# Optimization experiments

Hardware: AMD Instinct MI355X
Metric: run time of the kernel (lower is better)

Reference implementation:

```python
import jax, jax.numpy as jnp
import numpy as np

# ---- static dims ----
B, L, V = 8, 512, 100000
E, NERD, COREFD = 100, 20, 20          # word / ner / coref embedding dims
H, DIS, REL, HT = 128, 20, 97, 512     # hidden, dis embed, relations, n_pairs
W, N, R, C = 512, 32, 8, 256           # DNC word len, cells, read heads, ctrl hidden
IN_SIZE = E + NERD + COREFD            # 140 == H + 12 (required by final_layer)
DNC_OUT = H + 12                        # 140
CTRL_IN = IN_SIZE + R * W               # 4236
MASK_MIN, EPS, CLIP = 0.1, 1e-6, 20.0
# interface vector layout: read keys, read strengths, write key, write strength,
# erase, write vec, free gates, alloc gate, write gate, read modes,
# write mask, read masks, fwd sharpness, bwd sharpness
XI_SIZES = [R*W, R, W, 1, W, W, R, 1, 1, 3*R, W, R*W, R, R]
XI = sum(XI_SIZES)


def setup_inputs():
    key = jax.random.key(0)
    ks = iter(jax.random.split(key, 40))
    def nrm(shape, s=0.02):
        return (jax.random.normal(next(ks), shape) * s).astype(jnp.float32)
    def ri(shape, hi):
        return jax.random.randint(next(ks), shape, 0, hi)
    return dict(
        context_idxs=ri((B, L), V),
        pos=ri((B, L), L),
        context_ner=ri((B, L), 7),
        context_char_idxs=ri((B, L, 16), 262),
        context_lens=jnp.full((B,), L, dtype=jnp.int32),
        h_mapping=jax.random.uniform(next(ks), (B, HT, L), jnp.float32) / L,
        t_mapping=jax.random.uniform(next(ks), (B, HT, L), jnp.float32) / L,
        relation_mask=jnp.ones((B, HT), jnp.float32),
        dis_h_2_t=ri((B, HT), 20),
        dis_t_2_h=ri((B, HT), 20),
        word_emb=nrm((V, E), 0.1),
        entity_emb=nrm((L, COREFD), 0.1),
        ner_emb=nrm((7, NERD), 0.1),
        dis_emb=nrm((20, DIS), 0.1),
        Wih0=nrm((CTRL_IN, 4*C)), Whh0=nrm((C, 4*C)), b0=jnp.zeros((4*C,), jnp.float32),
        Wih1=nrm((C, 4*C)), Whh1=nrm((C, 4*C)), b1=jnp.zeros((4*C,), jnp.float32),
        Wih2=nrm((C, 4*C)), Whh2=nrm((C, 4*C)), b2=jnp.zeros((4*C,), jnp.float32),
        W_xi=nrm((C, XI)), b_xi=jnp.zeros((XI,), jnp.float32),
        W_out=nrm((C + R*W, DNC_OUT)), b_out=jnp.zeros((DNC_OUT,), jnp.float32),
        W_final=nrm((DNC_OUT, 2*H)), b_final=jnp.zeros((2*H,), jnp.float32),
        W_re=nrm((2*H, H)), b_re=jnp.zeros((H,), jnp.float32),
        W_bili=nrm((REL, H+DIS, H+DIS)), b_bili=jnp.zeros((REL,), jnp.float32),
    )


def _lstm(x, h, c, Wih, Whh, b):
    z = x @ Wih + h @ Whh + b
    i, f, g, o = jnp.split(z, 4, axis=-1)
    c = jax.nn.sigmoid(f) * c + jax.nn.sigmoid(i) * jnp.tanh(g)
    h = jax.nn.sigmoid(o) * jnp.tanh(c)
    return h, c


def _content(M, key_, beta, mask):
    # M [B,N,W]; key_, mask [B,h,W]; beta [B,h] -> weights [B,h,N]
    k = key_ * mask
    Mm = M[:, None] * mask[:, :, None]                 # [B,h,N,W]
    dot = jnp.einsum('bhw,bhnw->bhn', k, Mm)
    kn = jnp.linalg.norm(k, axis=-1)[..., None]
    Mn = jnp.linalg.norm(Mm, axis=-1)
    cos = dot / (kn * Mn + EPS)
    return jax.nn.softmax(beta[..., None] * cos, axis=-1)


def _sharpen(w, s):
    w = (w + EPS) ** s[..., None]
    return w / w.sum(-1, keepdims=True)


def _dnc(x, params):
    (Wih0, Whh0, b0, Wih1, Whh1, b1, Wih2, Whh2, b2, W_xi, b_xi, W_out, b_out) = params
    Bs = x.shape[0]
    eye = jnp.eye(N, dtype=x.dtype)
    splits = np.cumsum(XI_SIZES)[:-1]

    def step(carry, x_t):
        (h0, c0, h1, c1, h2, c2, M, u, wr, ww, p, Lnk, reads) = carry
        ci = jnp.concatenate([x_t, reads.reshape(Bs, R*W)], -1)
        h0, c0 = _lstm(ci, h0, c0, Wih0, Whh0, b0)
        h1, c1 = _lstm(h0, h1, c1, Wih1, Whh1, b1)
        h2, c2 = _lstm(h1, h2, c2, Wih2, Whh2, b2)
        h = jnp.clip(h2, -CLIP, CLIP)
        xi = h @ W_xi + b_xi
        (rk, rb, wk, wb, er, wv, fg, ga, gw, rm,
         wmask, rmask, sf, sb) = jnp.split(xi, splits, axis=-1)
        rk = rk.reshape(Bs, R, W)
        rb = 1 + jax.nn.softplus(rb)                    # [B,R]
        wk = wk.reshape(Bs, 1, W)
        wb = 1 + jax.nn.softplus(wb)                    # [B,1]
        er = jax.nn.sigmoid(er)                         # [B,W]
        fg = jax.nn.sigmoid(fg)                         # [B,R]
        ga = jax.nn.sigmoid(ga)
        gw = jax.nn.sigmoid(gw)
        pi = jax.nn.softmax(rm.reshape(Bs, R, 3), -1)
        wmask = MASK_MIN + (1 - MASK_MIN) * jax.nn.sigmoid(wmask)
        rmask = MASK_MIN + (1 - MASK_MIN) * jax.nn.sigmoid(rmask).reshape(Bs, R, W)
        sf = 1 + jax.nn.softplus(sf)
        sb = 1 + jax.nn.softplus(sb)

        # retention / usage
        psi = jnp.prod(1 - fg[:, :, None] * wr, axis=1)  # [B,N]
        u = (u + ww - u * ww) * psi
        # allocation weighting via sorted free list
        order = jnp.argsort(u, axis=-1)
        us = jnp.take_along_axis(u, order, -1)
        cp = jnp.cumprod(jnp.concatenate([jnp.ones((Bs, 1), u.dtype), us[:, :-1]], -1), -1)
        a_s = (1 - us) * cp
        a = jnp.zeros_like(u).at[jnp.arange(Bs)[:, None], order].set(a_s)
        # write addressing (masked content + allocation)
        cw = _content(M, wk, wb, wmask[:, None, :])[:, 0]
        ww = gw * (ga * a + (1 - ga) * cw)
        # de-allocate content of freed cells, then write
        M = M * psi[:, :, None]
        M = M * (1 - ww[:, :, None] * er[:, None, :]) + ww[:, :, None] * wv[:, None, :]
        # temporal link matrix (uses previous precedence p)
        Lnk = (1 - ww[:, :, None] - ww[:, None, :]) * Lnk + ww[:, :, None] * p[:, None, :]
        Lnk = Lnk * (1 - eye)
        p = (1 - ww.sum(-1, keepdims=True)) * p + ww
        # read addressing with link sharpness control
        fw = _sharpen(jnp.einsum('bij,brj->bri', Lnk, wr), sf)
        bw = _sharpen(jnp.einsum('bji,brj->bri', Lnk, wr), sb)
        cr = _content(M, rk, rb, rmask)
        wr = pi[..., 0:1] * bw + pi[..., 1:2] * cr + pi[..., 2:3] * fw
        reads = jnp.einsum('brn,bnw->brw', wr, M)
        y = jnp.concatenate([h, reads.reshape(Bs, R*W)], -1) @ W_out + b_out
        return (h0, c0, h1, c1, h2, c2, M, u, wr, ww, p, Lnk, reads), y

    z = jnp.zeros
    carry0 = (z((Bs, C)), z((Bs, C)), z((Bs, C)), z((Bs, C)), z((Bs, C)), z((Bs, C)),
              z((Bs, N, W)), z((Bs, N)), z((Bs, R, N)), z((Bs, N)), z((Bs, N)),
              z((Bs, N, N)), z((Bs, R, W)))
    _, ys = jax.lax.scan(step, carry0, x.transpose(1, 0, 2))
    return ys.transpose(1, 0, 2)  # [B,L,DNC_OUT]


def reference(context_idxs, pos, context_ner, context_char_idxs, context_lens,
              h_mapping, t_mapping, relation_mask, dis_h_2_t, dis_t_2_h,
              word_emb, entity_emb, ner_emb, dis_emb,
              Wih0, Whh0, b0, Wih1, Whh1, b1, Wih2, Whh2, b2,
              W_xi, b_xi, W_out, b_out, W_final, b_final, W_re, b_re,
              W_bili, b_bili):
    sent = jnp.concatenate([word_emb[context_idxs], entity_emb[pos],
                            ner_emb[context_ner]], -1)      # [B,L,140]
    dnc_params = (Wih0, Whh0, b0, Wih1, Whh1, b1, Wih2, Whh2, b2,
                  W_xi, b_xi, W_out, b_out)
    out = _dnc(sent, dnc_params)                             # [B,L,140]
    out = out @ W_final + b_final                            # LockedDropout: identity (eval)
    ctx = jax.nn.relu(out @ W_re + b_re)                     # [B,L,H]
    s0 = jnp.einsum('bpl,blh->bph', h_mapping, ctx)
    t0 = jnp.einsum('bpl,blh->bph', t_mapping, ctx)
    s_rep = jnp.concatenate([s0, dis_emb[dis_h_2_t]], -1)    # [B,P,148]
    t_rep = jnp.concatenate([t0, dis_emb[dis_t_2_h]], -1)
    return jnp.einsum('bpi,kij,bpj->bpk', s_rep, W_bili, t_rep) + b_bili
```

## Files before the change

kernel.cpp:

```cpp
#include <hip/hip_runtime.h>
#include <math.h>

#define B8      8
#define LSEQ    512
#define NWG     256
#define TPB     512
#define RELK    97
#define BI      148
#define FSTR    16

#define oWA     0
#define oW1     18432
#define oW2     20480
#define oWX     22528
#define oWY     34816
#define oST     37196
#define LDSF    40948
#define LDSB    (LDSF*4)

__device__ __forceinline__ float sigf(float x){
  return (x >= 0.f) ? 1.f/(1.f + expf(-x)) : expf(x)/(1.f + expf(x));
}
__device__ __forceinline__ float spf(float x){
  return (x > 0.f) ? x + log1pf(expf(-x)) : log1pf(expf(x));
}
__device__ __forceinline__ float agld(const float* p){
  return __hip_atomic_load(p, __ATOMIC_RELAXED, __HIP_MEMORY_SCOPE_AGENT);
}
__device__ __forceinline__ void agst(float* p, float v){
  __hip_atomic_store(p, v, __ATOMIC_RELAXED, __HIP_MEMORY_SCOPE_AGENT);
}

__global__ __launch_bounds__(256)
void k_sent(const int* __restrict__ cidx, const int* __restrict__ pos,
            const int* __restrict__ ner, const float* __restrict__ wemb,
            const float* __restrict__ eemb, const float* __restrict__ nemb,
            float* __restrict__ sent)
{
  int flat = blockIdx.x*256 + threadIdx.x;
  if (flat >= B8*LSEQ*140) return;
  int d = flat % 140; int bl = flat / 140;
  float v;
  if (d < 100)      v = wemb[(size_t)cidx[bl]*100 + d];
  else if (d < 120) v = eemb[(size_t)pos[bl]*20 + (d-100)];
  else              v = nemb[(size_t)ner[bl]*20 + (d-120)];
  sent[flat] = v;
}

__global__ __launch_bounds__(256)
void k_tr(const float* __restrict__ A, const float* __restrict__ Bsrc,
          int N, int K1a, int K1b, int K2, long long total, float* __restrict__ T)
{
  long long i = (long long)blockIdx.x*256 + threadIdx.x;
  if (i >= total) return;
  int k = (int)(i % K2);
  long long c = i / K2;
  float v = 0.f;
  if (k < K1a)            v = A[(size_t)k*N + c];
  else if (k < K1a+K1b)   v = Bsrc[(size_t)(k-K1a)*N + c];
  T[i] = v;
}

__device__ __forceinline__ void gbar(int* flags, int* genrep, int seq){
  __syncthreads();
  const int tid = threadIdx.x;
  const int bid = blockIdx.x;
  if (tid == 0){
    asm volatile("s_waitcnt vmcnt(0)" ::: "memory");
    __hip_atomic_store(&flags[bid*FSTR], seq, __ATOMIC_RELAXED, __HIP_MEMORY_SCOPE_AGENT);
  }
  if (bid == 0){
    if (tid < NWG){
      while (__hip_atomic_load(&flags[tid*FSTR], __ATOMIC_RELAXED, __HIP_MEMORY_SCOPE_AGENT) < seq)
        __builtin_amdgcn_s_sleep(1);
    }
    __syncthreads();
    if (tid < NWG)
      __hip_atomic_store(&genrep[tid*FSTR], seq, __ATOMIC_RELAXED, __HIP_MEMORY_SCOPE_AGENT);
  } else if (tid == 0){
    while (__hip_atomic_load(&genrep[bid*FSTR], __ATOMIC_RELAXED, __HIP_MEMORY_SCOPE_AGENT) < seq)
      __builtin_amdgcn_s_sleep(1);
  }
  __syncthreads();
}

__device__ void mem_phase(float* lds, const float* __restrict__ xi,
                          float* __restrict__ M, float* u_g, float* ww_g,
                          float* p_g, float* wr_g, float* L_g, float* rout)
{
  const int tid = threadIdx.x;
  float* mL  = lds;
  float* mwr = lds+1024;
  float* mwrn= lds+1280;
  float* mcr = lds+1536;
  float* mfw = lds+1792;
  float* mbw = lds+2048;
  float* PSI = lds+2304;
  float* UU  = lds+2336;
  float* US  = lds+2368;
  float* AA  = lds+2400;
  float* CW  = lds+2432;
  float* WWN = lds+2464;
  float* WWO = lds+2496;
  float* PP  = lds+2528;
  int*   mord= (int*)(lds+2560);
  float* mh  = lds+2592;
  float* mpi = lds+2624;
  float* msc = lds+2648;
  float* q1  = lds+2688;
  float* q2  = lds+3200;

  if (tid < 8){
    mh[tid]    = 1.f + spf(agld(&xi[4096+tid]));
    mh[8+tid]  = 1.f + spf(agld(&xi[10283+tid]));
    mh[16+tid] = 1.f + spf(agld(&xi[10291+tid]));
    mh[24+tid] = sigf(agld(&xi[5641+tid]));
    float e0=agld(&xi[5651+3*tid]), e1=agld(&xi[5652+3*tid]), e2=agld(&xi[5653+3*tid]);
    float mx=fmaxf(e0,fmaxf(e1,e2));
    float x0=expf(e0-mx), x1=expf(e1-mx), x2=expf(e2-mx);
    float inv=1.f/(x0+x1+x2);
    mpi[tid*3]=x0*inv; mpi[tid*3+1]=x1*inv; mpi[tid*3+2]=x2*inv;
  }
  if (tid==0){ msc[0]=1.f+spf(agld(&xi[4616])); msc[1]=sigf(agld(&xi[5649])); msc[2]=sigf(agld(&xi[5650])); }
  if (tid<32){ UU[tid]=u_g[tid]; WWO[tid]=ww_g[tid]; PP[tid]=p_g[tid]; }
  if (tid<256) mwr[tid]=wr_g[tid];
  mL[tid]=L_g[tid]; mL[tid+512]=L_g[tid+512];
  { float wm = 0.1f+0.9f*sigf(agld(&xi[5675+tid])); q1[tid]=agld(&xi[4104+tid])*wm; q2[tid]=wm; }
  __syncthreads();

  if (tid<32){
    float psi=1.f;
    #pragma unroll
    for (int r=0;r<8;r++) psi *= (1.f - mh[24+r]*mwr[r*32+tid]);
    PSI[tid]=psi;
    float uo=UU[tid], wo=WWO[tid];
    UU[tid]=(uo+wo-uo*wo)*psi;
  }
  __syncthreads();
  if (tid<32){
    float un=UU[tid]; int rank=0;
    for (int m=0;m<32;m++){ float um=UU[m]; rank += (um<un)||(um==un && m<tid); }
    mord[rank]=tid;
  }
  __syncthreads();
  if (tid<32) US[tid]=UU[mord[tid]];
  __syncthreads();
  if (tid==0){ float cp=1.f; for (int j=0;j<32;j++){ AA[mord[j]]=(1.f-US[j])*cp; cp*=US[j]; } }
  __syncthreads();

  { float q=q1[tid]*q1[tid];
    for (int o=32;o;o>>=1) q += __shfl_down(q,o,64);
    if ((tid&63)==0) msc[8+(tid>>6)]=q; }
  __syncthreads();
  if (tid==0){ float q=0.f; for (int i=0;i<8;i++) q+=msc[8+i]; msc[3]=sqrtf(q); }
  __syncthreads();
  { int n=tid>>4, wsub=tid&15;
    float d=0.f,q=0.f;
    for (int i=0;i<32;i++){ int w=wsub+16*i; float m=M[(size_t)n*512+w]; float t2=m*q2[w]; d+=q1[w]*t2; q+=t2*t2; }
    for (int o=8;o;o>>=1){ d+=__shfl_down(d,o,16); q+=__shfl_down(q,o,16); }
    if (wsub==0){ float cs=d/(msc[3]*sqrtf(q)+1e-6f); CW[n]=msc[0]*cs; } }
  __syncthreads();
  if (tid==0){ float mx=-1e30f; for(int n=0;n<32;n++) mx=fmaxf(mx,CW[n]); msc[4]=mx; }
  __syncthreads();
  if (tid<32) CW[tid]=expf(CW[tid]-msc[4]);
  __syncthreads();
  if (tid==0){ float sm=0.f; for(int n=0;n<32;n++) sm+=CW[n]; msc[5]=1.f/sm; }
  __syncthreads();
  if (tid<32) CW[tid]*=msc[5];
  __syncthreads();
  if (tid<32) WWN[tid]=msc[2]*(msc[1]*AA[tid]+(1.f-msc[1])*CW[tid]);
  __syncthreads();
  { float er=sigf(agld(&xi[4617+tid])); float wv=agld(&xi[5129+tid]);
    for (int n=0;n<32;n++){ size_t idx=(size_t)n*512+tid; float m=M[idx];
      M[idx]=m*PSI[n]*(1.f-WWN[n]*er)+WWN[n]*wv; } }
  __syncthreads();
  for (int ii=0;ii<2;ii++){ int f=tid+512*ii; int i=f>>5, j=f&31;
    float nl=(1.f-WWN[i]-WWN[j])*mL[f]+WWN[i]*PP[j];
    mL[f]=(i==j)?0.f:nl; }
  __syncthreads();
  if (tid==0){ float sw=0.f; for(int n=0;n<32;n++) sw+=WWN[n]; msc[6]=sw; }
  __syncthreads();
  if (tid<32) PP[tid]=(1.f-msc[6])*PP[tid]+WWN[tid];
  __syncthreads();
  { int r=(tid>>5)&7, i=tid&31; bool isB=(tid>=256);
    float accv=0.f;
    if (!isB){ for (int j=0;j<32;j++) accv += mL[i*32+j]*mwr[r*32+j]; }
    else     { for (int j=0;j<32;j++) accv += mL[j*32+i]*mwr[r*32+j]; }
    float sp = isB? mh[16+r] : mh[8+r];
    float e = expf(sp*logf(accv+1e-6f));
    if (!isB) mfw[r*32+i]=e; else mbw[r*32+i]=e; }
  __syncthreads();
  if (tid<16){ int r=tid&7; float sm=0.f;
    if (tid<8){ for(int n=0;n<32;n++) sm+=mfw[r*32+n]; msc[16+r]=1.f/sm; }
    else      { for(int n=0;n<32;n++) sm+=mbw[r*32+n]; msc[24+r]=1.f/sm; } }
  __syncthreads();
  { int r=(tid>>5)&7, i=tid&31; bool isB=(tid>=256);
    if (!isB) mfw[r*32+i]*=msc[16+r]; else mbw[r*32+i]*=msc[24+r]; }
  __syncthreads();
  for (int r=0;r<8;r++){
    { float rm=0.1f+0.9f*sigf(agld(&xi[6187+r*512+tid]));
      q1[tid]=agld(&xi[r*512+tid])*rm; q2[tid]=rm; }
    __syncthreads();
    { float q=q1[tid]*q1[tid];
      for (int o=32;o;o>>=1) q+=__shfl_down(q,o,64);
      if ((tid&63)==0) msc[8+(tid>>6)]=q; }
    __syncthreads();
    if (tid==0){ float qq=0.f; for(int i=0;i<8;i++) qq+=msc[8+i]; msc[32]=sqrtf(qq); }
    __syncthreads();
    { int n=tid>>4, wsub=tid&15;
      float d=0.f,q=0.f;
      for (int i=0;i<32;i++){ int w=wsub+16*i; float m=M[(size_t)n*512+w]; float t2=m*q2[w]; d+=q1[w]*t2; q+=t2*t2; }
      for (int o=8;o;o>>=1){ d+=__shfl_down(d,o,16); q+=__shfl_down(q,o,16); }
      if (wsub==0){ float cs=d/(msc[32]*sqrtf(q)+1e-6f); mcr[r*32+n]=mh[r]*cs; } }
    __syncthreads();
  }
  if (tid<8){ int r=tid; float mx=-1e30f;
    for (int n=0;n<32;n++) mx=fmaxf(mx,mcr[r*32+n]);
    float sm=0.f;
    for (int n=0;n<32;n++){ float e=expf(mcr[r*32+n]-mx); mcr[r*32+n]=e; sm+=e; }
    float inv=1.f/sm;
    for (int n=0;n<32;n++) mcr[r*32+n]*=inv; }
  __syncthreads();
  if (tid<256){ int r=tid>>5, n=tid&31;
    float v=mpi[r*3]*mbw[r*32+n]+mpi[r*3+1]*mcr[r*32+n]+mpi[r*3+2]*mfw[r*32+n];
    mwrn[tid]=v; wr_g[tid]=v; }
  __syncthreads();
  { int r=tid>>6, wsub=tid&63;
    for (int i2=0;i2<8;i2++){ int w=wsub+64*i2;
      float accv=0.f;
      for (int n=0;n<32;n++) accv+=mwrn[r*32+n]*M[(size_t)n*512+w];
      agst(&rout[r*512+w], accv); } }
  if (tid<32){ u_g[tid]=UU[tid]; ww_g[tid]=WWN[tid]; p_g[tid]=PP[tid]; }
  L_g[tid]=mL[tid]; L_g[tid+512]=mL[tid+512];
}

__global__ __launch_bounds__(TPB, 1)
void dnc_persist(
  const float* __restrict__ sent,
  const float* __restrict__ Wih0, const float* __restrict__ Whh0, const float* __restrict__ b0,
  const float* __restrict__ Wih1, const float* __restrict__ Whh1, const float* __restrict__ b1,
  const float* __restrict__ Wih2, const float* __restrict__ Whh2, const float* __restrict__ b2,
  const float* __restrict__ WXIT, const float* __restrict__ bxi,
  const float* __restrict__ Wout, const float* __restrict__ bout,
  float* __restrict__ yh,
  float* __restrict__ reads,
  float* __restrict__ h0, float* __restrict__ h1,
  float* __restrict__ h2u, float* __restrict__ h2c,
  float* __restrict__ c0p, float* __restrict__ c1p, float* __restrict__ c2p,
  float* __restrict__ zp0, float* __restrict__ zp1, float* __restrict__ zp2,
  float* __restrict__ yp, float* __restrict__ xig,
  float* __restrict__ Mb, float* __restrict__ ug, float* __restrict__ wwg,
  float* __restrict__ pg, float* __restrict__ wrg, float* __restrict__ Lg,
  int* flags, int* genrep)
{
  extern __shared__ float lds[];
  const int wg  = blockIdx.x;
  const int tid = threadIdx.x;
  const int cg  = wg >> 4, kg  = wg & 15;
  const int cgB = wg >> 3, kgB = wg & 7;
  const int ycg = wg >> 6, ykg = wg & 63;
  const int xc  = tid >> 6, xk = tid & 63;
  float* stg = lds + oST;
  int seq = 0;

  for (int f=tid; f<18432; f+=TPB){
    int kk=f>>6, cc=f&63;
    int gk=kg*288+kk, gc=cg*64+cc;
    float v=0.f;
    if (gk<4236) v=Wih0[(size_t)gk*1024+gc];
    else if (gk<4492) v=Whh0[(size_t)(gk-4236)*1024+gc];
    lds[oWA+f]=v;
  }
  for (int f=tid; f<2048; f+=TPB){
    int kk=f>>5, cc=f&31;
    int gk=kgB*64+kk, gc=cgB*32+cc;
    lds[oW1+f] = (gk<256)? Wih1[(size_t)gk*1024+gc] : Whh1[(size_t)(gk-256)*1024+gc];
  }
  for (int f=tid; f<2048; f+=TPB){
    int kk=f>>5, cc=f&31;
    int gk=kgB*64+kk, gc=cgB*32+cc;
    lds[oW2+f] = (gk<256)? Wih2[(size_t)gk*1024+gc] : Whh2[(size_t)(gk-256)*1024+gc];
  }
  for (int f=tid; f<12288; f+=TPB){
    int cl=f>>8, k=f&255; int col=wg*48+cl;
    lds[oWX+f] = (col<10299)? WXIT[(size_t)col*256+k] : 0.f;
  }
  for (int f=tid; f<2380; f+=TPB){
    int kk=f/35, cc=f%35;
    int gk=ykg*68+kk, gc=ycg*35+cc;
    lds[oWY+f] = Wout[(size_t)gk*140+gc];
  }
  __syncthreads();

  #pragma unroll 1
  for (int t=0; t<LSEQ; t++){
    {
      float* sAct = stg;
      float* sActY= stg+2304;
      for (int f=tid; f<2304; f+=TPB){
        int s=f/288, kk=f%288; int g=kg*288+kk;
        float v;
        if (g<140)       v = sent[((size_t)s*512+t)*140+g];
        else if (g<4236) v = agld(&reads[s*4096+g-140]);
        else if (g<4492) v = agld(&h0[s*256+(g-4236)]);
        else             v = 0.f;
        sAct[f]=v;
      }
      if (t>0) for (int f=tid; f<544; f+=TPB){
        int s=f/68, kk=f%68; int gy=ykg*68+kk;
        sActY[f] = (gy<256)? agld(&h2c[s*256+gy]) : agld(&reads[s*4096+gy-256]);
      }
      __syncthreads();
      { int cc=tid&63, s=tid>>6;
        const float* wAl = lds+oWA;
        const float* ac  = sAct + s*288;
        float acc=0.f;
        #pragma unroll 8
        for (int kk=0; kk<288; kk++) acc += wAl[kk*64+cc]*ac[kk];
        agst(&zp0[(size_t)(kg*8+s)*1024 + cg*64+cc], acc); }
      if (t>0 && tid<280){ int s=tid/35, cc=tid%35;
        const float* wYl = lds+oWY;
        const float* ac  = sActY + s*68;
        float acc=0.f;
        #pragma unroll 4
        for (int kk=0; kk<68; kk++) acc += wYl[kk*35+cc]*ac[kk];
        agst(&yp[(size_t)(ykg*8+s)*144 + ycg*35+cc], acc); }
    }
    gbar(flags,genrep,++seq);

    if (wg < 64){
      int s = wg>>3, part = wg&7;
      float* sP = stg;
      { int j32=tid&31, q=(tid>>5)&3, kp=tid>>7;
        int col = q*256 + part*32 + j32;
        float v=0.f;
        for (int k2=kp*4; k2<kp*4+4; k2++) v += agld(&zp0[(size_t)(k2*8+s)*1024+col]);
        sP[kp*128 + q*32 + j32] = v; }
      __syncthreads();
      if (tid<32){
        int j = part*32 + tid;
        float zq[4];
        #pragma unroll
        for (int q=0;q<4;q++){ float v=0.f;
          for (int k2=0;k2<4;k2++) v += sP[k2*128+q*32+tid];
          zq[q]=v + b0[q*256+j]; }
        float cold=c0p[s*256+j];
        float cn=sigf(zq[1])*cold + sigf(zq[0])*tanhf(zq[2]);
        float h=sigf(zq[3])*tanhf(cn);
        c0p[s*256+j]=cn;
        agst(&h0[s*256+j], h);
      }
    }
    gbar(flags,genrep,++seq);

    {
      float* sAct = stg;
      for (int f=tid; f<512; f+=TPB){ int s=f>>6, kk=f&63; int g=kgB*64+kk;
        sAct[f] = (g<256)? agld(&h0[s*256+g]) : agld(&h1[s*256+g-256]); }
      __syncthreads();
      if (tid<256){ int cc=tid&31, s=tid>>5;
        const float* w1l = lds+oW1;
        const float* ac  = sAct + s*64;
        float acc=0.f;
        #pragma unroll 8
        for (int kk=0; kk<64; kk++) acc += w1l[kk*32+cc]*ac[kk];
        agst(&zp1[(size_t)(kgB*8+s)*1024 + cgB*32+cc], acc); }
    }
    gbar(flags,genrep,++seq);

    if (wg < 64){
      int s = wg>>3, part = wg&7;
      float* sP = stg;
      if (tid<256){ int j32=tid&31, q=(tid>>5)&3, kp=tid>>7;
        int col = q*256 + part*32 + j32;
        float v=0.f;
        for (int k2=kp*4; k2<kp*4+4; k2++) v += agld(&zp1[(size_t)(k2*8+s)*1024+col]);
        sP[kp*128 + q*32 + j32] = v; }
      __syncthreads();
      if (tid<32){
        int j = part*32 + tid;
        float zq[4];
        #pragma unroll
        for (int q=0;q<4;q++) zq[q]=sP[q*32+tid]+sP[128+q*32+tid]+b1[q*256+j];
        float cold=c1p[s*256+j];
        float cn=sigf(zq[1])*cold + sigf(zq[0])*tanhf(zq[2]);
        float h=sigf(zq[3])*tanhf(cn);
        c1p[s*256+j]=cn;
        agst(&h1[s*256+j], h);
      }
    }
    gbar(flags,genrep,++seq);

    {
      float* sAct = stg;
      for (int f=tid; f<512; f+=TPB){ int s=f>>6, kk=f&63; int g=kgB*64+kk;
        sAct[f] = (g<256)? agld(&h1[s*256+g]) : agld(&h2u[s*256+g-256]); }
      __syncthreads();
      if (tid<256){ int cc=tid&31, s=tid>>5;
        const float* w2l = lds+oW2;
        const float* ac  = sAct + s*64;
        float acc=0.f;
        #pragma unroll 8
        for (int kk=0; kk<64; kk++) acc += w2l[kk*32+cc]*ac[kk];
        agst(&zp2[(size_t)(kgB*8+s)*1024 + cgB*32+cc], acc); }
    }
    gbar(flags,genrep,++seq);

    if (wg < 64){
      int s = wg>>3, part = wg&7;
      float* sP = stg;
      if (tid<256){ int j32=tid&31, q=(tid>>5)&3, kp=tid>>7;
        int col = q*256 + part*32 + j32;
        float v=0.f;
        for (int k2=kp*4; k2<kp*4+4; k2++) v += agld(&zp2[(size_t)(k2*8+s)*1024+col]);
        sP[kp*128 + q*32 + j32] = v; }
      __syncthreads();
      if (tid<32){
        int j = part*32 + tid;
        float zq[4];
        #pragma unroll
        for (int q=0;q<4;q++) zq[q]=sP[q*32+tid]+sP[128+q*32+tid]+b2[q*256+j];
        float cold=c2p[s*256+j];
        float cn=sigf(zq[1])*cold + sigf(zq[0])*tanhf(zq[2]);
        float h2=sigf(zq[3])*tanhf(cn);
        float hc=fminf(fmaxf(h2,-20.f),20.f);
        c2p[s*256+j]=cn;
        agst(&h2u[s*256+j], h2);
        agst(&h2c[s*256+j], hc);
      }
    }
    gbar(flags,genrep,++seq);

    {
      float* sA2 = stg;
      for (int f=tid; f<2048; f+=TPB){ int s=f>>8, j=f&255;
        sA2[s*260+j] = agld(&h2c[s*256+j]); }
      __syncthreads();
      float accx[6][8];
      #pragma unroll
      for (int cc=0;cc<6;cc++)
        #pragma unroll
        for (int s=0;s<8;s++) accx[cc][s]=0.f;
      #pragma unroll
      for (int s=0;s<8;s++){
        float4 a = *reinterpret_cast<const float4*>(&sA2[s*260 + (xk<<2)]);
        #pragma unroll
        for (int cc=0;cc<6;cc++){
          float4 wv = *reinterpret_cast<const float4*>(&lds[oWX + (xc*6+cc)*256 + (xk<<2)]);
          accx[cc][s] += a.x*wv.x + a.y*wv.y + a.z*wv.z + a.w*wv.w;
        }
      }
      #pragma unroll
      for (int o=32;o;o>>=1)
        #pragma unroll
        for (int cc=0;cc<6;cc++)
          #pragma unroll
          for (int s=0;s<8;s++) accx[cc][s]+=__shfl_down(accx[cc][s],o,64);
      if ((tid&63)==0){
        #pragma unroll
        for (int cc=0;cc<6;cc++){
          int col = wg*48 + xc*6 + cc;
          if (col < 10299){
            #pragma unroll
            for (int s=0;s<8;s++) agst(&xig[(size_t)s*10299+col], accx[cc][s]+bxi[col]);
          }
        }
      }
    }
    gbar(flags,genrep,++seq);

    if (wg < 8){
      mem_phase(stg, xig + (size_t)wg*10299, Mb + (size_t)wg*16384,
                ug+wg*32, wwg+wg*32, pg+wg*32, wrg+wg*256, Lg+wg*1024,
                reads + wg*4096);
    } else if (wg < 148 && t > 0){
      int ty = t-1, j = wg-8;
      int s = tid>>6, kg2 = tid&63;
      float v = agld(&yp[(size_t)(kg2*8+s)*144 + j]);
      #pragma unroll
      for (int o=32;o;o>>=1) v += __shfl_down(v,o,64);
      if (kg2==0) yh[((size_t)s*512+ty)*140+j] = v + bout[j];
    }
    gbar(flags,genrep,++seq);
  }

  {
    float* sActY = stg;
    for (int f=tid; f<544; f+=TPB){
      int s=f/68, kk=f%68; int gy=ykg*68+kk;
      sActY[f] = (gy<256)? agld(&h2c[s*256+gy]) : agld(&reads[s*4096+gy-256]);
    }
    __syncthreads();
    if (tid<280){ int s=tid/35, cc=tid%35;
      const float* wYl = lds+oWY;
      const float* ac  = sActY + s*68;
      float acc=0.f;
      for (int kk=0; kk<68; kk++) acc += wYl[kk*35+cc]*ac[kk];
      agst(&yp[(size_t)(ykg*8+s)*144 + ycg*35+cc], acc); }
  }
  gbar(flags,genrep,++seq);
  if (wg>=8 && wg<148){
    int j = wg-8;
    int s = tid>>6, kg2 = tid&63;
    float v = agld(&yp[(size_t)(kg2*8+s)*144 + j]);
    #pragma unroll
    for (int o=32;o;o>>=1) v += __shfl_down(v,o,64);
    if (kg2==0) yh[((size_t)s*512+511)*140+j] = v + bout[j];
  }
}

__global__ __launch_bounds__(256)
void gemm16(int M, int N, int K,
            const float* __restrict__ A, long long sAb, int lda,
            const float* __restrict__ Bm, long long sBb, int ldb,
            float* __restrict__ C, long long sCb, int ldc,
            const float* __restrict__ bias, int relu)
{
  __shared__ float sAh[16*512];
  const int tid = threadIdx.x;
  const float* Ab = A + (size_t)blockIdx.y*sAb;
  const float* Bb = Bm + (size_t)blockIdx.y*sBb;
  float* Cb = C + (size_t)blockIdx.y*sCb;
  const int m0 = blockIdx.x*16;
  const int tot = 16*K;
  for (int f = tid; f < tot; f += 256) sAh[f] = Ab[(size_t)m0*lda + f];
  __syncthreads();
  int c = (tid & 63)*4; int rg = tid >> 6;
  if (c >= N) return;
  float acc[4][4] = {};
  for (int k=0;k<K;k++){
    float4 bv = *reinterpret_cast<const float4*>(Bb + (size_t)k*ldb + c);
    #pragma unroll
    for (int rr=0;rr<4;rr++){
      float a = sAh[(rg*4+rr)*K + k];
      acc[rr][0] += a*bv.x; acc[rr][1] += a*bv.y; acc[rr][2] += a*bv.z; acc[rr][3] += a*bv.w;
    }
  }
  for (int rr=0;rr<4;rr++){
    int m = m0 + rg*4 + rr;
    #pragma unroll
    for (int e=0;e<4;e++){
      float v = acc[rr][e] + (bias ? bias[c+e] : 0.f);
      if (relu) v = fmaxf(v, 0.f);
      Cb[(size_t)m*ldc + c + e] = v;
    }
  }
}

__global__ __launch_bounds__(256)
void bilin(const float* __restrict__ s0, const float* __restrict__ t0,
           const float* __restrict__ dis_emb, const int* __restrict__ dht,
           const int* __restrict__ dth, const float* __restrict__ Wb,
           const float* __restrict__ bb, float* __restrict__ out)
{
  __shared__ float sS[BI][33];
  __shared__ float sT[32][152];
  const int tid = threadIdx.x;
  const int bp0 = blockIdx.x*32;
  for (int f = tid; f < 32*BI; f += 256){
    int pp = f / BI, i = f % BI;
    int bp = bp0 + pp;
    float sv, tv;
    if (i < 128){ sv = s0[(size_t)bp*128 + i]; tv = t0[(size_t)bp*128 + i]; }
    else {
      sv = dis_emb[(size_t)dht[bp]*20 + (i-128)];
      tv = dis_emb[(size_t)dth[bp]*20 + (i-128)];
    }
    sS[i][pp] = sv; sT[pp][i] = tv;
  }
  __syncthreads();
  const int ppg = tid >> 5, jb = tid & 31;
  const int pp0 = ppg*4;
  const int k0 = blockIdx.y*49, kend = min(k0+49, RELK);
  for (int k = k0; k < kend; k++){
    const float* Wk = Wb + (size_t)k*BI*BI;
    float acc[4][5];
    #pragma unroll
    for (int a=0;a<4;a++) for (int b=0;b<5;b++) acc[a][b]=0.f;
    for (int i=0;i<BI;i++){
      float sv0 = sS[i][pp0], sv1 = sS[i][pp0+1], sv2 = sS[i][pp0+2], sv3 = sS[i][pp0+3];
      const float* wrow = Wk + i*BI;
      #pragma unroll
      for (int jj=0;jj<5;jj++){
        int j = jb + 32*jj;
        if (j < BI){
          float w = wrow[j];
          acc[0][jj] += sv0*w; acc[1][jj] += sv1*w; acc[2][jj] += sv2*w; acc[3][jj] += sv3*w;
        }
      }
    }
    float dot[4] = {0.f,0.f,0.f,0.f};
    #pragma unroll
    for (int jj=0;jj<5;jj++){
      int j = jb + 32*jj;
      if (j < BI){
        #pragma unroll
        for (int p4=0;p4<4;p4++) dot[p4] += acc[p4][jj]*sT[pp0+p4][j];
      }
    }
    #pragma unroll
    for (int p4=0;p4<4;p4++)
      for (int o=16;o;o>>=1) dot[p4] += __shfl_down(dot[p4], o, 32);
    if (jb == 0){
      #pragma unroll
      for (int p4=0;p4<4;p4++)
        out[(size_t)(bp0+pp0+p4)*RELK + k] = dot[p4] + bb[k];
    }
  }
}

extern "C" void kernel_launch(void* const* d_in, const int* in_sizes, int n_in,
                              void* d_out, int out_size, void* d_ws, size_t ws_size,
                              hipStream_t stream)
{
  (void)in_sizes; (void)n_in; (void)out_size; (void)ws_size;
  const int*   ctx_idx = (const int*)  d_in[0];
  const int*   pos     = (const int*)  d_in[1];
  const int*   nerI    = (const int*)  d_in[2];
  const float* h_map   = (const float*)d_in[5];
  const float* t_map   = (const float*)d_in[6];
  const int*   dht     = (const int*)  d_in[8];
  const int*   dth     = (const int*)  d_in[9];
  const float* wemb    = (const float*)d_in[10];
  const float* eemb    = (const float*)d_in[11];
  const float* nemb    = (const float*)d_in[12];
  const float* demb    = (const float*)d_in[13];
  const float* Wih0    = (const float*)d_in[14];
  const float* Whh0    = (const float*)d_in[15];
  const float* b0      = (const float*)d_in[16];
  const float* Wih1    = (const float*)d_in[17];
  const float* Whh1    = (const float*)d_in[18];
  const float* b1      = (const float*)d_in[19];
  const float* Wih2    = (const float*)d_in[20];
  const float* Whh2    = (const float*)d_in[21];
  const float* b2      = (const float*)d_in[22];
  const float* Wxi     = (const float*)d_in[23];
  const float* bxi     = (const float*)d_in[24];
  const float* Wout    = (const float*)d_in[25];
  const float* bout    = (const float*)d_in[26];
  const float* Wfin    = (const float*)d_in[27];
  const float* bfin    = (const float*)d_in[28];
  const float* Wre     = (const float*)d_in[29];
  const float* bre     = (const float*)d_in[30];
  const float* Wbili   = (const float*)d_in[31];
  const float* bbili   = (const float*)d_in[32];

  float* ws    = (float*)d_ws;
  float* sent  = ws;
  float* yh    = sent + 573440;
  float* o256  = yh + 573440;
  float* s0b   = o256 + 1048576;
  float* t0b   = s0b + 524288;
  float* SB    = t0b + 524288;
  float* reads = SB + 0;
  float* h0    = SB + 32768;
  float* h1    = SB + 34816;
  float* h2u   = SB + 36864;
  float* h2c   = SB + 38912;
  float* c0p   = SB + 40960;
  float* c1p   = SB + 43008;
  float* c2p   = SB + 45056;
  float* zp0   = SB + 47104;
  float* zp1   = SB + 178176;
  float* zp2   = SB + 243712;
  float* yp    = SB + 309248;
  float* xig   = SB + 382976;
  float* Mb    = SB + 465368;
  float* ug    = SB + 596440;
  float* wwg   = SB + 596696;
  float* pg    = SB + 596952;
  float* wrg   = SB + 597208;
  float* Lg    = SB + 599256;
  float* barf  = SB + 607448;
  float* SEnd  = SB + 615640;
  float* WXIT  = SEnd;
  float* ctxb  = yh;
  int* flags  = (int*)barf;
  int* genrep = flags + 256*FSTR;

  hipMemsetAsync(SB, 0, (size_t)615640*sizeof(float), stream);

  hipLaunchKernelGGL(k_tr, dim3(10299), dim3(256), 0, stream,
                     Wxi, Wxi, 10299, 256, 0, 256, (long long)2636544, WXIT);
  hipLaunchKernelGGL(k_sent, dim3((573440+255)/256), dim3(256), 0, stream,
                     ctx_idx, pos, nerI, wemb, eemb, nemb, sent);

  hipFuncSetAttribute(reinterpret_cast<const void*>(dnc_persist),
                      hipFuncAttributeMaxDynamicSharedMemorySize, LDSB);

  hipLaunchKernelGGL(dnc_persist, dim3(NWG), dim3(TPB), LDSB, stream,
                     sent, Wih0, Whh0, b0, Wih1, Whh1, b1, Wih2, Whh2, b2,
                     WXIT, bxi, Wout, bout, yh, reads,
                     h0, h1, h2u, h2c, c0p, c1p, c2p,
                     zp0, zp1, zp2, yp, xig,
                     Mb, ug, wwg, pg, wrg, Lg, flags, genrep);

  hipLaunchKernelGGL(gemm16, dim3(256,1), dim3(256), 0, stream,
                     4096, 256, 140, yh, (long long)0, 140, Wfin, (long long)0, 256,
                     o256, (long long)0, 256, bfin, 0);
  hipLaunchKernelGGL(gemm16, dim3(256,1), dim3(256), 0, stream,
                     4096, 128, 256, o256, (long long)0, 256, Wre, (long long)0, 128,
                     ctxb, (long long)0, 128, bre, 1);
  hipLaunchKernelGGL(gemm16, dim3(32,8), dim3(256), 0, stream,
                     512, 128, 512, h_map, (long long)(512*512), 512,
                     ctxb, (long long)(512*128), 128,
                     s0b, (long long)(512*128), 128, (const float*)nullptr, 0);
  hipLaunchKernelGGL(gemm16, dim3(32,8), dim3(256), 0, stream,
                     512, 128, 512, t_map, (long long)(512*512), 512,
                     ctxb, (long long)(512*128), 128,
                     t0b, (long long)(512*128), 128, (const float*)nullptr, 0);
  hipLaunchKernelGGL(bilin, dim3(128,2), dim3(256), 0, stream,
                     s0b, t0b, demb, dht, dth, Wbili, bbili, (float*)d_out);
}
```

Measured before the change: 90.09 ms.

## Fuse LSTM layer 1/2 matvec with gate update per workgroup, cutting grid barriers

Each workgroup now owns one hidden unit across all four gates. It keeps the layer-1 and layer-2 weight columns in registers and computes the full dot product with wave shuffle reductions. This removes the partial-sum buffers zp1/zp2 and two grid-wide barriers per timestep. Layer-0 gate reduction also moves to shuffles across all 256 workgroups. h1/h2u are double-buffered to avoid read/write races, and the barrier spin sleep is lengthened. The cost is 64 extra VGPRs per thread for the weights and a larger sleep granularity, which may add barrier wake-up latency.

```diff
diff --git a/kernel.cpp b/kernel.cpp
--- a/kernel.cpp
+++ b/kernel.cpp
@@ -10,12 +10,10 @@
 #define FSTR    16
 
 #define oWA     0
-#define oW1     18432
-#define oW2     20480
-#define oWX     22528
-#define oWY     34816
-#define oST     37196
-#define LDSF    40948
+#define oWX     18432
+#define oWY     30720
+#define oST     33100
+#define LDSF    36852
 #define LDSB    (LDSF*4)
 
 __device__ __forceinline__ float sigf(float x){
@@ -72,14 +70,14 @@
   if (bid == 0){
     if (tid < NWG){
       while (__hip_atomic_load(&flags[tid*FSTR], __ATOMIC_RELAXED, __HIP_MEMORY_SCOPE_AGENT) < seq)
-        __builtin_amdgcn_s_sleep(1);
+        __builtin_amdgcn_s_sleep(8);
     }
     __syncthreads();
     if (tid < NWG)
       __hip_atomic_store(&genrep[tid*FSTR], seq, __ATOMIC_RELAXED, __HIP_MEMORY_SCOPE_AGENT);
   } else if (tid == 0){
     while (__hip_atomic_load(&genrep[bid*FSTR], __ATOMIC_RELAXED, __HIP_MEMORY_SCOPE_AGENT) < seq)
-      __builtin_amdgcn_s_sleep(1);
+      __builtin_amdgcn_s_sleep(8);
   }
   __syncthreads();
 }
@@ -247,7 +245,7 @@
   float* __restrict__ h0, float* __restrict__ h1,
   float* __restrict__ h2u, float* __restrict__ h2c,
   float* __restrict__ c0p, float* __restrict__ c1p, float* __restrict__ c2p,
-  float* __restrict__ zp0, float* __restrict__ zp1, float* __restrict__ zp2,
+  float* __restrict__ zp0,
   float* __restrict__ yp, float* __restrict__ xig,
   float* __restrict__ Mb, float* __restrict__ ug, float* __restrict__ wwg,
   float* __restrict__ pg, float* __restrict__ wrg, float* __restrict__ Lg,
@@ -257,9 +255,9 @@
   const int wg  = blockIdx.x;
   const int tid = threadIdx.x;
   const int cg  = wg >> 4, kg  = wg & 15;
-  const int cgB = wg >> 3, kgB = wg & 7;
   const int ycg = wg >> 6, ykg = wg & 63;
   const int xc  = tid >> 6, xk = tid & 63;
+  const int lane = tid & 63, sw = tid >> 6;
   float* stg = lds + oST;
   int seq = 0;
 
@@ -271,16 +269,6 @@
     else if (gk<4492) v=Whh0[(size_t)(gk-4236)*1024+gc];
     lds[oWA+f]=v;
   }
-  for (int f=tid; f<2048; f+=TPB){
-    int kk=f>>5, cc=f&31;
-    int gk=kgB*64+kk, gc=cgB*32+cc;
-    lds[oW1+f] = (gk<256)? Wih1[(size_t)gk*1024+gc] : Whh1[(size_t)(gk-256)*1024+gc];
-  }
-  for (int f=tid; f<2048; f+=TPB){
-    int kk=f>>5, cc=f&31;
-    int gk=kgB*64+kk, gc=cgB*32+cc;
-    lds[oW2+f] = (gk<256)? Wih2[(size_t)gk*1024+gc] : Whh2[(size_t)(gk-256)*1024+gc];
-  }
   for (int f=tid; f<12288; f+=TPB){
     int cl=f>>8, k=f&255; int col=wg*48+cl;
     lds[oWX+f] = (col<10299)? WXIT[(size_t)col*256+k] : 0.f;
@@ -290,10 +278,28 @@
     int gk=ykg*68+kk, gc=ycg*35+cc;
     lds[oWY+f] = Wout[(size_t)gk*140+gc];
   }
+  float w1r[32], w2r[32];
+  #pragma unroll
+  for (int g=0; g<4; g++)
+    #pragma unroll
+    for (int i=0; i<8; i++){
+      int kk = lane + 64*i;
+      w1r[g*8+i] = (kk<256)? Wih1[(size_t)kk*1024 + g*256+wg]
+                           : Whh1[(size_t)(kk-256)*1024 + g*256+wg];
+      w2r[g*8+i] = (kk<256)? Wih2[(size_t)kk*1024 + g*256+wg]
+                           : Whh2[(size_t)(kk-256)*1024 + g*256+wg];
+    }
+  float bb0[4], bb1[4], bb2[4];
+  #pragma unroll
+  for (int g=0; g<4; g++){
+    bb0[g]=b0[g*256+wg]; bb1[g]=b1[g*256+wg]; bb2[g]=b2[g*256+wg];
+  }
   __syncthreads();
 
   #pragma unroll 1
   for (int t=0; t<LSEQ; t++){
+    const int hb = t&1, hw = hb^1;
+
     {
       float* sAct = stg;
       float* sActY= stg+2304;
@@ -328,105 +334,79 @@
     }
     gbar(flags,genrep,++seq);
 
-    if (wg < 64){
-      int s = wg>>3, part = wg&7;
-      float* sP = stg;
-      { int j32=tid&31, q=(tid>>5)&3, kp=tid>>7;
-        int col = q*256 + part*32 + j32;
-        float v=0.f;
-        for (int k2=kp*4; k2<kp*4+4; k2++) v += agld(&zp0[(size_t)(k2*8+s)*1024+col]);
-        sP[kp*128 + q*32 + j32] = v; }
-      __syncthreads();
-      if (tid<32){
-        int j = part*32 + tid;
-        float zq[4];
-        #pragma unroll
-        for (int q=0;q<4;q++){ float v=0.f;
-          for (int k2=0;k2<4;k2++) v += sP[k2*128+q*32+tid];
-          zq[q]=v + b0[q*256+j]; }
-        float cold=c0p[s*256+j];
-        float cn=sigf(zq[1])*cold + sigf(zq[0])*tanhf(zq[2]);
-        float h=sigf(zq[3])*tanhf(cn);
-        c0p[s*256+j]=cn;
-        agst(&h0[s*256+j], h);
+    {
+      int g = lane>>4, p = lane&15;
+      float val = agld(&zp0[(size_t)(p*8+sw)*1024 + g*256 + wg]);
+      #pragma unroll
+      for (int o=8;o;o>>=1) val += __shfl_down(val,o,16);
+      float zi=__shfl(val, 0,64), zf=__shfl(val,16,64);
+      float zg=__shfl(val,32,64), zo=__shfl(val,48,64);
+      if (lane==0){
+        zi+=bb0[0]; zf+=bb0[1]; zg+=bb0[2]; zo+=bb0[3];
+        float cold=c0p[sw*256+wg];
+        float cn=sigf(zf)*cold + sigf(zi)*tanhf(zg);
+        float h=sigf(zo)*tanhf(cn);
+        c0p[sw*256+wg]=cn;
+        agst(&h0[sw*256+wg], h);
       }
     }
     gbar(flags,genrep,++seq);
 
     {
-      float* sAct = stg;
-      for (int f=tid; f<512; f+=TPB){ int s=f>>6, kk=f&63; int g=kgB*64+kk;
-        sAct[f] = (g<256)? agld(&h0[s*256+g]) : agld(&h1[s*256+g-256]); }
-      __syncthreads();
-      if (tid<256){ int cc=tid&31, s=tid>>5;
-        const float* w1l = lds+oW1;
-        const float* ac  = sAct + s*64;
-        float acc=0.f;
-        #pragma unroll 8
-        for (int kk=0; kk<64; kk++) acc += w1l[kk*32+cc]*ac[kk];
-        agst(&zp1[(size_t)(kgB*8+s)*1024 + cgB*32+cc], acc); }
+      const float* h1r = h1 + (size_t)hb*2048;
+      float a[8];
+      #pragma unroll
+      for (int i=0;i<8;i++){
+        int k = lane + 64*i;
+        a[i] = (i<4)? agld(&h0[sw*256+k]) : agld(&h1r[sw*256+k-256]);
+      }
+      float acc[4]={0.f,0.f,0.f,0.f};
+      #pragma unroll
+      for (int i=0;i<8;i++)
+        #pragma unroll
+        for (int g=0;g<4;g++) acc[g] += a[i]*w1r[g*8+i];
+      #pragma unroll
+      for (int o=32;o;o>>=1)
+        #pragma unroll
+        for (int g=0;g<4;g++) acc[g]+=__shfl_down(acc[g],o,64);
+      if (lane==0){
+        float zi=acc[0]+bb1[0], zf=acc[1]+bb1[1], zg=acc[2]+bb1[2], zo=acc[3]+bb1[3];
+        float cold=c1p[sw*256+wg];
+        float cn=sigf(zf)*cold + sigf(zi)*tanhf(zg);
+        float h=sigf(zo)*tanhf(cn);
+        c1p[sw*256+wg]=cn;
+        agst(&h1[(size_t)hw*2048 + sw*256+wg], h);
+      }
     }
     gbar(flags,genrep,++seq);
 
-    if (wg < 64){
-      int s = wg>>3, part = wg&7;
-      float* sP = stg;
-      if (tid<256){ int j32=tid&31, q=(tid>>5)&3, kp=tid>>7;
-        int col = q*256 + part*32 + j32;
-        float v=0.f;
-        for (int k2=kp*4; k2<kp*4+4; k2++) v += agld(&zp1[(size_t)(k2*8+s)*1024+col]);
-        sP[kp*128 + q*32 + j32] = v; }
-      __syncthreads();
-      if (tid<32){
-        int j = part*32 + tid;
-        float zq[4];
-        #pragma unroll
-        for (int q=0;q<4;q++) zq[q]=sP[q*32+tid]+sP[128+q*32+tid]+b1[q*256+j];
-        float cold=c1p[s*256+j];
-        float cn=sigf(zq[1])*cold + sigf(zq[0])*tanhf(zq[2]);
-        float h=sigf(zq[3])*tanhf(cn);
-        c1p[s*256+j]=cn;
-        agst(&h1[s*256+j], h);
-      }
-    }
-    gbar(flags,genrep,++seq);
-
     {
-      float* sAct = stg;
-      for (int f=tid; f<512; f+=TPB){ int s=f>>6, kk=f&63; int g=kgB*64+kk;
-        sAct[f] = (g<256)? agld(&h1[s*256+g]) : agld(&h2u[s*256+g-256]); }
-      __syncthreads();
-      if (tid<256){ int cc=tid&31, s=tid>>5;
-        const float* w2l = lds+oW2;
-        const float* ac  = sAct + s*64;
-        float acc=0.f;
-        #pragma unroll 8
-        for (int kk=0; kk<64; kk++) acc += w2l[kk*32+cc]*ac[kk];
-        agst(&zp2[(size_t)(kgB*8+s)*1024 + cgB*32+cc], acc); }
-    }
-    gbar(flags,genrep,++seq);
-
-    if (wg < 64){
-      int s = wg>>3, part = wg&7;
-      float* sP = stg;
-      if (tid<256){ int j32=tid&31, q=(tid>>5)&3, kp=tid>>7;
-        int col = q*256 + part*32 + j32;
-        float v=0.f;
-        for (int k2=kp*4; k2<kp*4+4; k2++) v += agld(&zp2[(size_t)(k2*8+s)*1024+col]);
-        sP[kp*128 + q*32 + j32] = v; }
-      __syncthreads();
-      if (tid<32){
-        int j = part*32 + tid;
-        float zq[4];
-        #pragma unroll
-        for (int q=0;q<4;q++) zq[q]=sP[q*32+tid]+sP[128+q*32+tid]+b2[q*256+j];
-        float cold=c2p[s*256+j];
-        float cn=sigf(zq[1])*cold + sigf(zq[0])*tanhf(zq[2]);
-        float h2=sigf(zq[3])*tanhf(cn);
+      const float* h1c = h1 + (size_t)hw*2048;
+      const float* h2r = h2u + (size_t)hb*2048;
+      float a[8];
+      #pragma unroll
+      for (int i=0;i<8;i++){
+        int k = lane + 64*i;
+        a[i] = (i<4)? agld(&h1c[sw*256+k]) : agld(&h2r[sw*256+k-256]);
+      }
+      float acc[4]={0.f,0.f,0.f,0.f};
+      #pragma unroll
+      for (int i=0;i<8;i++)
+        #pragma unroll
+        for (int g=0;g<4;g++) acc[g] += a[i]*w2r[g*8+i];
+      #pragma unroll
+      for (int o=32;o;o>>=1)
+        #pragma unroll
+        for (int g=0;g<4;g++) acc[g]+=__shfl_down(acc[g],o,64);
+      if (lane==0){
+        float zi=acc[0]+bb2[0], zf=acc[1]+bb2[1], zg=acc[2]+bb2[2], zo=acc[3]+bb2[3];
+        float cold=c2p[sw*256+wg];
+        float cn=sigf(zf)*cold + sigf(zi)*tanhf(zg);
+        float h2=sigf(zo)*tanhf(cn);
         float hc=fminf(fmaxf(h2,-20.f),20.f);
-        c2p[s*256+j]=cn;
-        agst(&h2u[s*256+j], h2);
-        agst(&h2c[s*256+j], hc);
+        c2p[sw*256+wg]=cn;
+        agst(&h2u[(size_t)hw*2048 + sw*256+wg], h2);
+        agst(&h2c[sw*256+wg], hc);
       }
     }
     gbar(flags,genrep,++seq);
@@ -655,30 +635,28 @@
   float* reads = SB + 0;
   float* h0    = SB + 32768;
   float* h1    = SB + 34816;
-  float* h2u   = SB + 36864;
-  float* h2c   = SB + 38912;
-  float* c0p   = SB + 40960;
-  float* c1p   = SB + 43008;
-  float* c2p   = SB + 45056;
-  float* zp0   = SB + 47104;
-  float* zp1   = SB + 178176;
-  float* zp2   = SB + 243712;
-  float* yp    = SB + 309248;
-  float* xig   = SB + 382976;
-  float* Mb    = SB + 465368;
-  float* ug    = SB + 596440;
-  float* wwg   = SB + 596696;
-  float* pg    = SB + 596952;
-  float* wrg   = SB + 597208;
-  float* Lg    = SB + 599256;
-  float* barf  = SB + 607448;
-  float* SEnd  = SB + 615640;
+  float* h2u   = SB + 38912;
+  float* h2c   = SB + 43008;
+  float* c0p   = SB + 45056;
+  float* c1p   = SB + 47104;
+  float* c2p   = SB + 49152;
+  float* zp0   = SB + 51200;
+  float* yp    = SB + 182272;
+  float* xig   = SB + 256000;
+  float* Mb    = SB + 338392;
+  float* ug    = SB + 469464;
+  float* wwg   = SB + 469720;
+  float* pg    = SB + 469976;
+  float* wrg   = SB + 470232;
+  float* Lg    = SB + 472280;
+  float* barf  = SB + 480472;
+  float* SEnd  = SB + 488664;
   float* WXIT  = SEnd;
   float* ctxb  = yh;
   int* flags  = (int*)barf;
   int* genrep = flags + 256*FSTR;
 
-  hipMemsetAsync(SB, 0, (size_t)615640*sizeof(float), stream);
+  hipMemsetAsync(SB, 0, (size_t)488664*sizeof(float), stream);
 
   hipLaunchKernelGGL(k_tr, dim3(10299), dim3(256), 0, stream,
                      Wxi, Wxi, 10299, 256, 0, 256, (long long)2636544, WXIT);
@@ -692,7 +670,7 @@
                      sent, Wih0, Whh0, b0, Wih1, Whh1, b1, Wih2, Whh2, b2,
                      WXIT, bxi, Wout, bout, yh, reads,
                      h0, h1, h2u, h2c, c0p, c1p, c2p,
-                     zp0, zp1, zp2, yp, xig,
+                     zp0, yp, xig,
                      Mb, ug, wwg, pg, wrg, Lg, flags, genrep);
 
   hipLaunchKernelGGL(gemm16, dim3(256,1), dim3(256), 0, stream,
```

After: 90.51 ms. No clear change (+0.5%).
